# Optimization experiments

Hardware: AMD Instinct MI355X
Metric: run time of the kernel (lower is better)

## Reference

```python
import jax, jax.numpy as jnp
import numpy as np

TIME_DECAY = 0.1
B, S, D = 2048, 200, 128
H1, H2 = 64, 32


def setup_inputs() -> dict:
    key = jax.random.key(0)
    ks = jax.random.split(key, 8)
    query = jax.random.normal(ks[0], (B, D), dtype=jnp.float32)
    keys = jax.random.normal(ks[1], (B, S, D), dtype=jnp.float32)
    keys_mask = jax.random.randint(ks[2], (B, S), 0, 2).astype(jnp.bool_)
    # Linear weights stored as [in, out] (torch uses [out, in] with x @ W.T; same math)
    W1 = jax.random.normal(ks[3], (4 * D, H1), dtype=jnp.float32) / np.sqrt(4 * D)
    b1 = jnp.zeros((H1,), dtype=jnp.float32)
    a1 = jnp.asarray(0.25, dtype=jnp.float32)  # PReLU default init
    W2 = jax.random.normal(ks[4], (H1, H2), dtype=jnp.float32) / np.sqrt(H1)
    b2 = jnp.zeros((H2,), dtype=jnp.float32)
    a2 = jnp.asarray(0.25, dtype=jnp.float32)
    W3 = jax.random.normal(ks[5], (H2, 1), dtype=jnp.float32) / np.sqrt(H2)
    b3 = jnp.zeros((1,), dtype=jnp.float32)
    return {"query": query, "keys": keys, "keys_mask": keys_mask,
            "W1": W1, "b1": b1, "a1": a1, "W2": W2, "b2": b2, "a2": a2,
            "W3": W3, "b3": b3}


def _prelu(x, a):
    return jnp.maximum(x, 0) + a * jnp.minimum(x, 0)


def reference(query, keys, keys_mask, W1, b1, a1, W2, b2, a2, W3, b3):
    b, s, d = keys.shape
    q = jnp.broadcast_to(query[:, None, :], (b, s, d))
    # [B, S, 4D] concat of feature interactions
    x = jnp.concatenate([keys, q, keys * q, keys - q], axis=-1)
    h = _prelu(x @ W1 + b1, a1)
    h = _prelu(h @ W2 + b2, a2)
    scores = (h @ W3 + b3)[..., 0]  # [B, S]
    pos = jnp.arange(s, dtype=scores.dtype)
    time_w = jnp.exp(TIME_DECAY * (pos - s + 1))  # [S]
    scores = scores * time_w[None, :]
    scores = jnp.where(keys_mask, scores, -jnp.inf)
    w = jax.nn.softmax(scores, axis=-1)
    w = jnp.where(jnp.isnan(w), jnp.zeros_like(w), w)  # all-masked rows -> 0
    weighted_sum = jnp.einsum('bs,bsd->bd', w, keys)
    return weighted_sum, w
```

## Files before the change

### kernel.cpp

```cpp
#include <hip/hip_runtime.h>
#include <math.h>

#define NB 2048
#define NS 200
#define ND 128

typedef __attribute__((ext_vector_type(8))) short bf16x8;
typedef __attribute__((ext_vector_type(4))) float f32x4;

#define U_W1T   0
#define U_W2T   8448
#define U_Q     10624
#define U_BIAS  10752
#define U_B2    10816
#define U_W3    10848
#define U_SC    10880
#define U_WB    11088
#define U_WRED  11296
#define U_BP    11304
#define U_TOTAL 11564

__device__ __forceinline__ unsigned int packsplit(float x) {
    unsigned int u  = __float_as_uint(x);
    unsigned int hb = u >> 16;
    float lof = x - __uint_as_float(hb << 16);
    return hb | (__float_as_uint(lof) & 0xFFFF0000u);
}

extern "C" __global__ void __launch_bounds__(256, 3)
tdra_main(const float* __restrict__ query,
          const float* __restrict__ keys,
          const int*   __restrict__ kmask,
          const float* __restrict__ W1,
          const float* __restrict__ b1,
          const float* __restrict__ a1p,
          const float* __restrict__ W2,
          const float* __restrict__ b2,
          const float* __restrict__ a2p,
          const float* __restrict__ W3,
          const float* __restrict__ b3p,
          float* __restrict__ out)
{
    __shared__ __align__(16) unsigned int smem[U_TOTAL];
    unsigned int* W1T = smem + U_W1T;
    unsigned int* W2T = smem + U_W2T;
    float* qf    = (float*)(smem + U_Q);
    float* biasE = (float*)(smem + U_BIAS);
    float* b2f   = (float*)(smem + U_B2);
    float* w3f   = (float*)(smem + U_W3);
    float* scf   = (float*)(smem + U_SC);
    float* wbf   = (float*)(smem + U_WB);
    float* wred  = (float*)(smem + U_WRED);
    float* bpf   = (float*)(smem + U_BP);

    const int tid = threadIdx.x;
    const int b   = blockIdx.x;
    const float a1 = a1p[0];
    const float a2 = a2p[0];
    const float b3 = b3p[0];

    if (tid < 32) {
        float4 qv = *(const float4*)(query + (size_t)b * ND + tid * 4);
        *(float4*)(qf + tid * 4) = qv;
    } else if (tid < 64) {
        b2f[tid - 32] = b2[tid - 32];
    } else if (tid < 96) {
        w3f[tid - 64] = W3[tid - 64];
    }
    {
        int j = tid & 31, hblk = tid >> 5;
        unsigned int pk[8];
        #pragma unroll
        for (int i = 0; i < 8; ++i)
            pk[i] = packsplit(W2[(hblk * 8 + i) * 32 + j]);
        unsigned int* dst = W2T + j * 68 + hblk * 8;
        *(uint4*)(dst)     = make_uint4(pk[0], pk[1], pk[2], pk[3]);
        *(uint4*)(dst + 4) = make_uint4(pk[4], pk[5], pk[6], pk[7]);
    }
    __syncthreads();

    {
        int h = tid & 63, dg = tid >> 6;
        #pragma unroll 2
        for (int i = 0; i < 8; ++i) {
            int dblk = dg * 8 + i;
            unsigned int pk[4];
            #pragma unroll
            for (int jj = 0; jj < 4; ++jj) {
                int d = dblk * 4 + jj;
                float qd = qf[d];
                float va = W1[d * 64 + h];
                float vc = W1[16384 + d * 64 + h];
                float vd = W1[24576 + d * 64 + h];
                pk[jj] = packsplit(va + vd + qd * vc);
            }
            *(uint4*)(W1T + h * 132 + dblk * 4) = make_uint4(pk[0], pk[1], pk[2], pk[3]);
        }
        int qt = dg;
        const float* pb = W1 + (size_t)(128 + qt * 32) * 64 + h;
        const float* pd = W1 + (size_t)(384 + qt * 32) * 64 + h;
        float p = 0.f;
        #pragma unroll 8
        for (int i = 0; i < 32; ++i)
            p = fmaf(qf[qt * 32 + i], pb[i * 64] - pd[i * 64], p);
        bpf[qt * 65 + h] = p;
    }
    __syncthreads();
    if (tid < 64)
        biasE[tid] = b1[tid] + bpf[tid] + bpf[65 + tid] + bpf[130 + tid] + bpf[195 + tid];
    __syncthreads();

    const int wv = tid >> 6;
    const int c  = tid & 15;
    const int G  = (tid >> 4) & 3;

    bf16x8 A2h[2][2], A2l[2][2];
    #pragma unroll
    for (int jt = 0; jt < 2; ++jt)
        #pragma unroll
        for (int kt = 0; kt < 2; ++kt) {
            const unsigned int* p2 = W2T + (jt * 16 + c) * 68 + kt * 32 + 8 * G;
            uint4 wa = *(const uint4*)p2;
            uint4 wb = *(const uint4*)(p2 + 4);
            unsigned int ww[8] = {wa.x, wa.y, wa.z, wa.w, wb.x, wb.y, wb.z, wb.w};
            #pragma unroll
            for (int e = 0; e < 8; ++e) {
                A2h[jt][kt][e] = (short)(ww[e] & 0xFFFFu);
                A2l[jt][kt][e] = (short)(ww[e] >> 16);
            }
        }

    float4 xs[8];
    {
        int row = wv * 16 + c; if (row > 199) row = 199;
        const float* kp = keys + ((size_t)b * NS + row) * ND + 8 * G;
        #pragma unroll
        for (int dt = 0; dt < 4; ++dt) {
            xs[2 * dt]     = *(const float4*)(kp + dt * 32);
            xs[2 * dt + 1] = *(const float4*)(kp + dt * 32 + 4);
        }
    }

    #pragma unroll 1
    for (int st = wv; st < 13; st += 4) {
        bf16x8 B1h[4], B1l[4];
        #pragma unroll
        for (int dt = 0; dt < 4; ++dt) {
            float t_[8] = {xs[2*dt].x, xs[2*dt].y, xs[2*dt].z, xs[2*dt].w,
                           xs[2*dt+1].x, xs[2*dt+1].y, xs[2*dt+1].z, xs[2*dt+1].w};
            #pragma unroll
            for (int e = 0; e < 8; ++e) {
                unsigned int u  = __float_as_uint(t_[e]);
                unsigned int hb = u >> 16;
                float lof = t_[e] - __uint_as_float(hb << 16);
                B1h[dt][e] = (short)hb;
                B1l[dt][e] = (short)(__float_as_uint(lof) >> 16);
            }
        }
        if (st + 4 < 13) {
            int row = (st + 4) * 16 + c; if (row > 199) row = 199;
            const float* kp = keys + ((size_t)b * NS + row) * ND + 8 * G;
            #pragma unroll
            for (int dt = 0; dt < 4; ++dt) {
                xs[2 * dt]     = *(const float4*)(kp + dt * 32);
                xs[2 * dt + 1] = *(const float4*)(kp + dt * 32 + 4);
            }
        }

        f32x4 acc1[4];
        #pragma unroll
        for (int ht = 0; ht < 4; ++ht)
            acc1[ht] = *(const f32x4*)(biasE + 16 * ht + 4 * G);
        #pragma unroll
        for (int dt = 0; dt < 4; ++dt) {
            #pragma unroll
            for (int ht = 0; ht < 4; ++ht) {
                const unsigned int* pa = W1T + (16 * ht + c) * 132 + dt * 32 + 8 * G;
                uint4 wa = *(const uint4*)pa;
                uint4 wb = *(const uint4*)(pa + 4);
                unsigned int ww[8] = {wa.x, wa.y, wa.z, wa.w, wb.x, wb.y, wb.z, wb.w};
                bf16x8 A1h, A1l;
                #pragma unroll
                for (int e = 0; e < 8; ++e) {
                    A1h[e] = (short)(ww[e] & 0xFFFFu);
                    A1l[e] = (short)(ww[e] >> 16);
                }
                acc1[ht] = __builtin_amdgcn_mfma_f32_16x16x32_bf16(A1h, B1h[dt], acc1[ht], 0, 0, 0);
                acc1[ht] = __builtin_amdgcn_mfma_f32_16x16x32_bf16(A1h, B1l[dt], acc1[ht], 0, 0, 0);
                acc1[ht] = __builtin_amdgcn_mfma_f32_16x16x32_bf16(A1l, B1h[dt], acc1[ht], 0, 0, 0);
            }
        }

        unsigned int p[4][4];
        #pragma unroll
        for (int ht = 0; ht < 4; ++ht)
            #pragma unroll
            for (int r = 0; r < 4; ++r) {
                float v = acc1[ht][r];
                v = fmaxf(v, 0.f) + a1 * fminf(v, 0.f);
                p[ht][r] = packsplit(v);
            }

        f32x4 acc2[2];
        acc2[0] = *(const f32x4*)(b2f + 4 * G);
        acc2[1] = *(const f32x4*)(b2f + 16 + 4 * G);
        const int srcbase = ((tid & 16) ? 32 : 0) + c;
        #pragma unroll
        for (int kt = 0; kt < 2; ++kt) {
            unsigned int q[8];
            #pragma unroll
            for (int half = 0; half < 2; ++half) {
                int src = srcbase + half * 16;
                #pragma unroll
                for (int r = 0; r < 4; ++r) {
                    unsigned int v0 = (unsigned int)__shfl((int)p[2 * kt][r], src, 64);
                    unsigned int v1 = (unsigned int)__shfl((int)p[2 * kt + 1][r], src, 64);
                    q[half * 4 + r] = (tid & 32) ? v1 : v0;
                }
            }
            bf16x8 B2h_, B2l_;
            #pragma unroll
            for (int e = 0; e < 8; ++e) {
                B2h_[e] = (short)(q[e] & 0xFFFFu);
                B2l_[e] = (short)(q[e] >> 16);
            }
            #pragma unroll
            for (int jt = 0; jt < 2; ++jt) {
                acc2[jt] = __builtin_amdgcn_mfma_f32_16x16x32_bf16(A2h[jt][kt], B2h_, acc2[jt], 0, 0, 0);
                acc2[jt] = __builtin_amdgcn_mfma_f32_16x16x32_bf16(A2h[jt][kt], B2l_, acc2[jt], 0, 0, 0);
                acc2[jt] = __builtin_amdgcn_mfma_f32_16x16x32_bf16(A2l[jt][kt], B2h_, acc2[jt], 0, 0, 0);
            }
        }

        float sv = 0.f;
        #pragma unroll
        for (int jt = 0; jt < 2; ++jt)
            #pragma unroll
            for (int r = 0; r < 4; ++r) {
                float v = acc2[jt][r];
                v = fmaxf(v, 0.f) + a2 * fminf(v, 0.f);
                sv = fmaf(v, w3f[jt * 16 + 4 * G + r], sv);
            }
        sv += __shfl_xor(sv, 16, 64);
        sv += __shfl_xor(sv, 32, 64);
        int srow = st * 16 + c;
        if ((tid & 48) == 0 && srow < NS) scf[srow] = sv + b3;
    }
    __syncthreads();

    float scval = -INFINITY;
    if (tid < NS) {
        if (kmask[(size_t)b * NS + tid] != 0)
            scval = scf[tid] * expf(0.1f * (float)(tid - (NS - 1)));
    }
    const int wid = tid >> 6, lane = tid & 63;
    float mx = scval;
    #pragma unroll
    for (int o = 32; o > 0; o >>= 1) mx = fmaxf(mx, __shfl_xor(mx, o, 64));
    if (lane == 0) wred[wid] = mx;
    __syncthreads();
    float M = fmaxf(fmaxf(wred[0], wred[1]), fmaxf(wred[2], wred[3]));
    float e = (M > -INFINITY) ? expf(scval - M) : 0.f;
    float ssum = e;
    #pragma unroll
    for (int o = 32; o > 0; o >>= 1) ssum += __shfl_xor(ssum, o, 64);
    if (lane == 0) wred[4 + wid] = ssum;
    __syncthreads();
    float SUM = wred[4] + wred[5] + wred[6] + wred[7];
    float wv_ = (SUM > 0.f) ? (e / SUM) : 0.f;
    if (tid < NS) {
        wbf[tid] = wv_;
        out[(size_t)NB * ND + (size_t)b * NS + tid] = wv_;
    }
    __syncthreads();

    {
        const int d = tid & 127, half = tid >> 7;
        const float* kp = keys + ((size_t)b * NS + half * 100) * ND + d;
        float pacc = 0.f;
        #pragma unroll 5
        for (int i = 0; i < 100; ++i)
            pacc = fmaf(wbf[half * 100 + i], kp[(size_t)i * ND], pacc);
        bpf[half * 128 + d] = pacc;
    }
    __syncthreads();
    if (tid < 128)
        out[(size_t)b * ND + tid] = bpf[tid] + bpf[128 + tid];
}

extern "C" void kernel_launch(void* const* d_in, const int* in_sizes, int n_in,
                              void* d_out, int out_size, void* d_ws, size_t ws_size,
                              hipStream_t stream) {
    (void)in_sizes; (void)n_in; (void)d_ws; (void)ws_size; (void)out_size;
    const float* query = (const float*)d_in[0];
    const float* keys  = (const float*)d_in[1];
    const int*   kmask = (const int*)d_in[2];
    const float* W1 = (const float*)d_in[3];
    const float* b1 = (const float*)d_in[4];
    const float* a1 = (const float*)d_in[5];
    const float* W2 = (const float*)d_in[6];
    const float* b2 = (const float*)d_in[7];
    const float* a2 = (const float*)d_in[8];
    const float* W3 = (const float*)d_in[9];
    const float* b3 = (const float*)d_in[10];
    float* out = (float*)d_out;

    hipLaunchKernelGGL(tdra_main, dim3(NB), dim3(256), 0, stream,
                       query, keys, kmask, W1, b1, a1, W2, b2, a2, W3, b3, out);
}
```

Baseline: 83.94 us.

## Split W1 hi/lo planes in LDS, load W2 from global, raise occupancy

Stores the folded W1 as separate hi and lo bf16 planes in shared memory so MFMA operands load directly as bf16x8 without unpacking. W2 fragments are now built straight from global memory into registers, which drops the W2T shared buffer and shrinks LDS. The keys register prefetch across loop iterations is removed in favor of in-iteration loads split into halves. Launch bounds are raised to 4 blocks per SM. Together these aim to cut register and LDS pressure and unpack ALU work in exchange for less latency hiding on the keys loads.

```diff
diff --git a/kernel.cpp b/kernel.cpp
--- a/kernel.cpp
+++ b/kernel.cpp
@@ -7,27 +7,21 @@
 
 typedef __attribute__((ext_vector_type(8))) short bf16x8;
 typedef __attribute__((ext_vector_type(4))) float f32x4;
-
-#define U_W1T   0
-#define U_W2T   8448
-#define U_Q     10624
-#define U_BIAS  10752
-#define U_B2    10816
-#define U_W3    10848
-#define U_SC    10880
-#define U_WB    11088
-#define U_WRED  11296
-#define U_BP    11304
-#define U_TOTAL 11564
-
-__device__ __forceinline__ unsigned int packsplit(float x) {
-    unsigned int u  = __float_as_uint(x);
-    unsigned int hb = u >> 16;
-    float lof = x - __uint_as_float(hb << 16);
-    return hb | (__float_as_uint(lof) & 0xFFFF0000u);
-}
-
-extern "C" __global__ void __launch_bounds__(256, 3)
+typedef __attribute__((ext_vector_type(4))) unsigned short u16x4;
+
+#define U_W1HI  0
+#define U_W1LO  4352
+#define U_Q     8704
+#define U_BIAS  8832
+#define U_B2    8896
+#define U_W3    8928
+#define U_SC    8960
+#define U_WB    9168
+#define U_WRED  9376
+#define U_BP    9384
+#define U_TOTAL 9644
+
+extern "C" __global__ void __launch_bounds__(256, 4)
 tdra_main(const float* __restrict__ query,
           const float* __restrict__ keys,
           const int*   __restrict__ kmask,
@@ -42,8 +36,8 @@
           float* __restrict__ out)
 {
     __shared__ __align__(16) unsigned int smem[U_TOTAL];
-    unsigned int* W1T = smem + U_W1T;
-    unsigned int* W2T = smem + U_W2T;
+    unsigned short* W1hi = (unsigned short*)(smem + U_W1HI);
+    unsigned short* W1lo = (unsigned short*)(smem + U_W1LO);
     float* qf    = (float*)(smem + U_Q);
     float* biasE = (float*)(smem + U_BIAS);
     float* b2f   = (float*)(smem + U_B2);
@@ -59,6 +53,10 @@
     const float a2 = a2p[0];
     const float b3 = b3p[0];
 
+    const int wv = tid >> 6;
+    const int c  = tid & 15;
+    const int G  = (tid >> 4) & 3;
+
     if (tid < 32) {
         float4 qv = *(const float4*)(query + (size_t)b * ND + tid * 4);
         *(float4*)(qf + tid * 4) = qv;
@@ -67,16 +65,21 @@
     } else if (tid < 96) {
         w3f[tid - 64] = W3[tid - 64];
     }
-    {
-        int j = tid & 31, hblk = tid >> 5;
-        unsigned int pk[8];
-        #pragma unroll
-        for (int i = 0; i < 8; ++i)
-            pk[i] = packsplit(W2[(hblk * 8 + i) * 32 + j]);
-        unsigned int* dst = W2T + j * 68 + hblk * 8;
-        *(uint4*)(dst)     = make_uint4(pk[0], pk[1], pk[2], pk[3]);
-        *(uint4*)(dst + 4) = make_uint4(pk[4], pk[5], pk[6], pk[7]);
-    }
+
+    bf16x8 A2h[2][2], A2l[2][2];
+    #pragma unroll
+    for (int jt = 0; jt < 2; ++jt)
+        #pragma unroll
+        for (int kt = 0; kt < 2; ++kt)
+            #pragma unroll
+            for (int e = 0; e < 8; ++e) {
+                float x = W2[(kt * 32 + 8 * G + e) * 32 + jt * 16 + c];
+                unsigned int u  = __float_as_uint(x);
+                unsigned int hb = u & 0xFFFF0000u;
+                float lof = x - __uint_as_float(hb);
+                A2h[jt][kt][e] = (short)(u >> 16);
+                A2l[jt][kt][e] = (short)(__float_as_uint(lof) >> 16);
+            }
     __syncthreads();
 
     {
@@ -84,7 +87,7 @@
         #pragma unroll 2
         for (int i = 0; i < 8; ++i) {
             int dblk = dg * 8 + i;
-            unsigned int pk[4];
+            u16x4 hi4, lo4;
             #pragma unroll
             for (int jj = 0; jj < 4; ++jj) {
                 int d = dblk * 4 + jj;
@@ -92,9 +95,15 @@
                 float va = W1[d * 64 + h];
                 float vc = W1[16384 + d * 64 + h];
                 float vd = W1[24576 + d * 64 + h];
-                pk[jj] = packsplit(va + vd + qd * vc);
-            }
-            *(uint4*)(W1T + h * 132 + dblk * 4) = make_uint4(pk[0], pk[1], pk[2], pk[3]);
+                float x  = va + vd + qd * vc;
+                unsigned int u  = __float_as_uint(x);
+                unsigned int hb = u & 0xFFFF0000u;
+                float lof = x - __uint_as_float(hb);
+                hi4[jj] = (unsigned short)(u >> 16);
+                lo4[jj] = (unsigned short)(__float_as_uint(lof) >> 16);
+            }
+            *(u16x4*)(W1hi + h * 136 + dblk * 4) = hi4;
+            *(u16x4*)(W1lo + h * 136 + dblk * 4) = lo4;
         }
         int qt = dg;
         const float* pb = W1 + (size_t)(128 + qt * 32) * 64 + h;
@@ -110,60 +119,33 @@
         biasE[tid] = b1[tid] + bpf[tid] + bpf[65 + tid] + bpf[130 + tid] + bpf[195 + tid];
     __syncthreads();
 
-    const int wv = tid >> 6;
-    const int c  = tid & 15;
-    const int G  = (tid >> 4) & 3;
-
-    bf16x8 A2h[2][2], A2l[2][2];
-    #pragma unroll
-    for (int jt = 0; jt < 2; ++jt)
-        #pragma unroll
-        for (int kt = 0; kt < 2; ++kt) {
-            const unsigned int* p2 = W2T + (jt * 16 + c) * 68 + kt * 32 + 8 * G;
-            uint4 wa = *(const uint4*)p2;
-            uint4 wb = *(const uint4*)(p2 + 4);
-            unsigned int ww[8] = {wa.x, wa.y, wa.z, wa.w, wb.x, wb.y, wb.z, wb.w};
-            #pragma unroll
-            for (int e = 0; e < 8; ++e) {
-                A2h[jt][kt][e] = (short)(ww[e] & 0xFFFFu);
-                A2l[jt][kt][e] = (short)(ww[e] >> 16);
-            }
-        }
-
-    float4 xs[8];
-    {
-        int row = wv * 16 + c; if (row > 199) row = 199;
-        const float* kp = keys + ((size_t)b * NS + row) * ND + 8 * G;
-        #pragma unroll
-        for (int dt = 0; dt < 4; ++dt) {
-            xs[2 * dt]     = *(const float4*)(kp + dt * 32);
-            xs[2 * dt + 1] = *(const float4*)(kp + dt * 32 + 4);
-        }
-    }
-
     #pragma unroll 1
     for (int st = wv; st < 13; st += 4) {
+        int row = st * 16 + c; if (row > 199) row = 199;
+        const float* kp = keys + ((size_t)b * NS + row) * ND + 8 * G;
+
         bf16x8 B1h[4], B1l[4];
         #pragma unroll
-        for (int dt = 0; dt < 4; ++dt) {
-            float t_[8] = {xs[2*dt].x, xs[2*dt].y, xs[2*dt].z, xs[2*dt].w,
-                           xs[2*dt+1].x, xs[2*dt+1].y, xs[2*dt+1].z, xs[2*dt+1].w};
-            #pragma unroll
-            for (int e = 0; e < 8; ++e) {
-                unsigned int u  = __float_as_uint(t_[e]);
-                unsigned int hb = u >> 16;
-                float lof = t_[e] - __uint_as_float(hb << 16);
-                B1h[dt][e] = (short)hb;
-                B1l[dt][e] = (short)(__float_as_uint(lof) >> 16);
-            }
-        }
-        if (st + 4 < 13) {
-            int row = (st + 4) * 16 + c; if (row > 199) row = 199;
-            const float* kp = keys + ((size_t)b * NS + row) * ND + 8 * G;
-            #pragma unroll
-            for (int dt = 0; dt < 4; ++dt) {
-                xs[2 * dt]     = *(const float4*)(kp + dt * 32);
-                xs[2 * dt + 1] = *(const float4*)(kp + dt * 32 + 4);
+        for (int half = 0; half < 2; ++half) {
+            float4 xs[4];
+            #pragma unroll
+            for (int q_ = 0; q_ < 2; ++q_) {
+                xs[2 * q_]     = *(const float4*)(kp + (2 * half + q_) * 32);
+                xs[2 * q_ + 1] = *(const float4*)(kp + (2 * half + q_) * 32 + 4);
+            }
+            #pragma unroll
+            for (int q_ = 0; q_ < 2; ++q_) {
+                int dt = 2 * half + q_;
+                float t_[8] = {xs[2*q_].x, xs[2*q_].y, xs[2*q_].z, xs[2*q_].w,
+                               xs[2*q_+1].x, xs[2*q_+1].y, xs[2*q_+1].z, xs[2*q_+1].w};
+                #pragma unroll
+                for (int e = 0; e < 8; ++e) {
+                    unsigned int u  = __float_as_uint(t_[e]);
+                    unsigned int hb = u & 0xFFFF0000u;
+                    float lof = t_[e] - __uint_as_float(hb);
+                    B1h[dt][e] = (short)(u >> 16);
+                    B1l[dt][e] = (short)(__float_as_uint(lof) >> 16);
+                }
             }
         }
 
@@ -175,16 +157,9 @@
         for (int dt = 0; dt < 4; ++dt) {
             #pragma unroll
             for (int ht = 0; ht < 4; ++ht) {
-                const unsigned int* pa = W1T + (16 * ht + c) * 132 + dt * 32 + 8 * G;
-                uint4 wa = *(const uint4*)pa;
-                uint4 wb = *(const uint4*)(pa + 4);
-                unsigned int ww[8] = {wa.x, wa.y, wa.z, wa.w, wb.x, wb.y, wb.z, wb.w};
-                bf16x8 A1h, A1l;
-                #pragma unroll
-                for (int e = 0; e < 8; ++e) {
-                    A1h[e] = (short)(ww[e] & 0xFFFFu);
-                    A1l[e] = (short)(ww[e] >> 16);
-                }
+                int idx = (16 * ht + c) * 136 + 32 * dt + 8 * G;
+                bf16x8 A1h = *(const bf16x8*)(W1hi + idx);
+                bf16x8 A1l = *(const bf16x8*)(W1lo + idx);
                 acc1[ht] = __builtin_amdgcn_mfma_f32_16x16x32_bf16(A1h, B1h[dt], acc1[ht], 0, 0, 0);
                 acc1[ht] = __builtin_amdgcn_mfma_f32_16x16x32_bf16(A1h, B1l[dt], acc1[ht], 0, 0, 0);
                 acc1[ht] = __builtin_amdgcn_mfma_f32_16x16x32_bf16(A1l, B1h[dt], acc1[ht], 0, 0, 0);
@@ -198,7 +173,10 @@
             for (int r = 0; r < 4; ++r) {
                 float v = acc1[ht][r];
                 v = fmaxf(v, 0.f) + a1 * fminf(v, 0.f);
-                p[ht][r] = packsplit(v);
+                unsigned int u  = __float_as_uint(v);
+                unsigned int hb = u & 0xFFFF0000u;
+                float lof = v - __uint_as_float(hb);
+                p[ht][r] = (u >> 16) | (__float_as_uint(lof) & 0xFFFF0000u);
             }
 
         f32x4 acc2[2];
```

Result: faster. 77.36 us (-7.8%).
